# Kernel tuning notes

Measured on AMD Instinct MI355X. Metric: run time of the kernel, lower is better.

Reference implementation:

```python
import jax, jax.numpy as jnp
import numpy as np

EPS = 1.0        # model eps for norm
STEP = 0.05      # step_size

def _norm(x):
    # torch: x / (eps + x.std(-1, keepdims=True)), torch std is unbiased (ddof=1)
    return x / (EPS + jnp.std(x, axis=-1, keepdims=True, ddof=1))

def setup_inputs() -> dict:
    key = jax.random.key(0)
    B, L, LM = 4, 512, 64
    G, E, K, D, KN = 32000, 256, 8, 6, 4
    ks = jax.random.split(key, 16)
    s = lambda k, shape, fan: (jax.random.normal(k, shape, jnp.float32) / np.sqrt(fan)).astype(jnp.float32)
    return dict(
        masked=jax.random.randint(ks[0], (B, L), 0, G),
        unmasked=jax.random.randint(ks[1], (B, L), 0, G),
        mask=jax.random.randint(ks[2], (B, LM), 0, L),
        embed=s(ks[3], (G, E), E),                 # embedding table
        Wt=s(ks[4], (D, E, E), E),                 # transition.weight per layer
        bt=jnp.zeros((D, E), jnp.float32),         # transition.bias per layer
        Wtc=s(ks[5], (D, E, E), E),                # transcore.weight per layer
        Wq=s(ks[6], (D, K * E, E), E),             # attq.weight per layer
        Wd=s(ks[7], (D, K * E, K * E), K * E),     # att_dense.weight per layer
        Wo=s(ks[8], (D, K * E, E), K * E),         # atto.weight per layer
        Wu=s(ks[9], (D, E, E), E),                 # updater.weight per layer
        Wem=s(ks[10], (E, E), E),                  # emittor.weight (head)
        Wkc=s(ks[11], (E * KN, E), E),             # kchoice.weight (head)
        bkc=jnp.zeros((E * KN,), jnp.float32),     # kchoice.bias (head)
    )

def reference(masked, unmasked, mask, embed, Wt, bt, Wtc, Wq, Wd, Wo, Wu, Wem, Wkc, bkc):
    B, L = masked.shape
    G, E = embed.shape
    K = Wq.shape[1] // E
    KN = Wkc.shape[0] // E
    inv_sqrt_e = 1.0 / np.sqrt(E)

    z = _norm(embed[masked])          # [B,L,E] input image
    xsa0 = z

    def step(xsa, p):
        wt, bt_, wtc, wq, wd, wo, wu = p
        # roll-based left/right transitions
        xsad = jax.nn.relu(jnp.roll(xsa, 1, axis=1) @ wt) @ wtc
        xsad = xsad + jax.nn.relu(jnp.roll(xsa, -1, axis=1) @ wtc.T) @ wt.T
        xsad = xsad + z @ wu.T + bt_   # use_input_image
        # QKV_Attention with kernel-expanded head dim: q [B,L,K,E] vs keys/values xsa [B,L,E]
        q = (xsa @ wq.T).reshape(B, L, K, E)
        h = jnp.einsum('blke,bme->blkm', q, xsa) * inv_sqrt_e
        pijk = jax.nn.softmax(h, axis=-1)
        y = jnp.einsum('blkm,bme->blke', pijk, xsa).reshape(B, L, K * E)
        # mode 1: Dense -> Relu -> Dense
        xid = jax.nn.relu(y @ wd.T) @ wo     # [B,L,E]
        xsad = _norm(xsad + xid)             # use_gradnorm
        xsa = _norm(xsa + STEP * xsad)       # use_layernorm
        return xsa, None

    xsa, _ = jax.lax.scan(step, xsa0, (Wt, bt, Wtc, Wq, Wd, Wo, Wu))

    # k-choice loss head (callback_cent)
    LM = mask.shape[1]
    lptok = jnp.take_along_axis(xsa, mask[:, :, None], axis=1)         # [B,LM,E]
    xx = (lptok @ Wkc.T + bkc).reshape(B, LM * KN, E)                  # kchoice
    xx = jnp.einsum('bnl,ble->bne', jnp.einsum('bne,ble->bnl', xx, xsa), xsa)
    logits = (xx @ Wem) @ embed.T                                      # [B,LM*KN,G]
    k_lp = jax.nn.log_softmax(logits, axis=-1).reshape(B, LM, KN, G)
    lptok = jax.scipy.special.logsumexp(k_lp, axis=2) - jnp.log(jnp.float32(KN))
    tgt = jnp.take_along_axis(unmasked, mask, axis=1)                  # [B,LM]
    cent = jnp.take_along_axis(lptok, tgt[:, :, None], axis=-1)[:, :, 0]
    return -cent.mean(-1)                                              # [B]
```

## Files before the change

kernel.cpp:

```cpp
#include <hip/hip_runtime.h>
#include <hip/hip_bf16.h>
#include <math.h>

typedef __bf16 bf16x8 __attribute__((ext_vector_type(8)));
typedef float floatx4 __attribute__((ext_vector_type(4)));

__device__ __forceinline__ short f2b(float f) {
  __hip_bfloat16 h = __float2bfloat16(f);
  return *reinterpret_cast<short*>(&h);
}
__device__ __forceinline__ float b2f(short s) {
  unsigned u = ((unsigned)(unsigned short)s) << 16;
  float f;
  __builtin_memcpy(&f, &u, 4);
  return f;
}

__device__ __forceinline__ void gl2lds16(const void* g, void* l) {
  __builtin_amdgcn_global_load_lds((__attribute__((address_space(1))) const void*)g,
                                   (__attribute__((address_space(3))) void*)l, 16, 0, 0);
}

__device__ __forceinline__ float block_sum(float v, float* sdata) {
#pragma unroll
  for (int o = 32; o > 0; o >>= 1) v += __shfl_down(v, o, 64);
  __syncthreads();
  int lane = threadIdx.x & 63, wid = threadIdx.x >> 6;
  if (lane == 0) sdata[wid] = v;
  __syncthreads();
  float s = 0.f;
  int nw = blockDim.x >> 6;
  for (int i = 0; i < nw; i++) s += sdata[i];
  return s;
}

__global__ void cvt_kernel(const float* __restrict__ src, short* __restrict__ dst, long n4) {
  long i = (long)blockIdx.x * blockDim.x + threadIdx.x;
  if (i < n4) {
    float4 v = ((const float4*)src)[i];
    short4 o;
    o.x = f2b(v.x); o.y = f2b(v.y); o.z = f2b(v.z); o.w = f2b(v.w);
    ((short4*)dst)[i] = o;
  }
}

__global__ void cvt2_kernel(const float* __restrict__ src, short* __restrict__ dst,
                            int ldS, int ldD, long sS, long sD) {
  src += (size_t)blockIdx.z * sS;
  dst += (size_t)blockIdx.z * sD;
  int c = blockIdx.x * 32 + threadIdx.x;
  int r0 = blockIdx.y * 32 + threadIdx.y;
#pragma unroll
  for (int i = 0; i < 32; i += 8)
    dst[(size_t)(r0 + i) * ldD + c] = f2b(src[(size_t)(r0 + i) * ldS + c]);
}

__global__ void cvtT2_kernel(const float* __restrict__ src, short* __restrict__ dst,
                             int ldS, int ldD, long sS, long sD) {
  src += (size_t)blockIdx.z * sS;
  dst += (size_t)blockIdx.z * sD;
  __shared__ float tile[32][33];
  int r0 = blockIdx.y * 32, c0 = blockIdx.x * 32;
  int tx = threadIdx.x, ty = threadIdx.y;
#pragma unroll
  for (int i = 0; i < 32; i += 8)
    tile[ty + i][tx] = src[(size_t)(r0 + ty + i) * ldS + c0 + tx];
  __syncthreads();
#pragma unroll
  for (int i = 0; i < 32; i += 8)
    dst[(size_t)(c0 + ty + i) * ldD + r0 + tx] = f2b(tile[tx][ty + i]);
}

__global__ void embed_norm_kernel(const int* __restrict__ masked,
                                  const float* __restrict__ embed,
                                  float* __restrict__ xsa, short* __restrict__ xsa_bf,
                                  short* __restrict__ xsaT_bf, short* __restrict__ t3,
                                  int E, int L) {
  int row = blockIdx.x;
  int g = masked[row];
  __shared__ float sdata[8];
  float x = embed[(size_t)g * E + threadIdx.x];
  float mean = block_sum(x, sdata) / E;
  float d = x - mean;
  float var = block_sum(d * d, sdata) / (E - 1);
  float val = x / (1.0f + sqrtf(var));
  size_t off = (size_t)row * E + threadIdx.x;
  xsa[off] = val;
  short b = f2b(val);
  xsa_bf[off] = b;
  t3[(size_t)row * 3 * E + 2 * E + threadIdx.x] = b;
  int bb = row / L, l = row - bb * L;
  xsaT_bf[((size_t)bb * E + threadIdx.x) * L + l] = b;
}

template <int BM, int BN, int OUT_BF16>
__global__ __launch_bounds__(256) void bgemm_kernel(
    const short* __restrict__ A, int lda, long sA,
    const short* __restrict__ B, int ldb, long sB,
    void* __restrict__ Cv, int ldc, long sC,
    int Ksz, float alpha, const float* __restrict__ bias,
    int relu, int shiftA, int shiftB, int nsplit, int Lroll) {
  constexpr int WM = BM / 2, WN = BN / 2;
  constexpr int MT = WM / 16, NT = WN / 16;
  constexpr int NCH = (BM + BN) * 8;
  constexpr int LPT = NCH / 256;
  A += (size_t)blockIdx.z * sA;
  B += (size_t)blockIdx.z * sB;
  float* Cf = (float*)Cv + (size_t)blockIdx.z * sC;
  short* Cb = (short*)Cv + (size_t)blockIdx.z * sC;
  int m0 = blockIdx.y * BM, n0 = blockIdx.x * BN;
  int shift = (n0 < nsplit) ? shiftA : shiftB;
  __shared__ short S[2][(BM + BN) * 64];
  int tid = threadIdx.x, lane = tid & 63, w = tid >> 6;
  int wm = (w & 1) * WM, wn = (w >> 1) * WN;
  int ml = lane & 15, q4 = lane >> 4, sw = ml & 7;

  const short* src[LPT];
#pragma unroll
  for (int i = 0; i < LPT; i++) {
    int q = i * 256 + w * 64 + lane;
    if (q < BM * 8) {
      int m = q >> 3, cl = q & 7, cs = cl ^ (m & 7);
      int mg = m0 + m;
      if (shift != 0) {
        int bb = mg / Lroll, l = mg - bb * Lroll;
        l = (l + shift + Lroll) % Lroll;
        mg = bb * Lroll + l;
      }
      src[i] = A + (size_t)mg * lda + cs * 8;
    } else {
      int qb = q - BM * 8;
      int n = qb >> 3, cl = qb & 7, cs = cl ^ (n & 7);
      src[i] = B + (size_t)(n0 + n) * ldb + cs * 8;
    }
  }
#pragma unroll
  for (int i = 0; i < LPT; i++)
    gl2lds16(src[i], &S[0][(i * 256 + w * 64) * 8]);
  floatx4 acc[MT][NT] = {};
  int nT = Ksz >> 6;
  for (int t = 0; t < nT; t++) {
    __syncthreads();
    int cur = t & 1;
    if (t + 1 < nT) {
      int nxt = cur ^ 1, ko = (t + 1) * 64;
#pragma unroll
      for (int i = 0; i < LPT; i++)
        gl2lds16(src[i] + ko, &S[nxt][(i * 256 + w * 64) * 8]);
    }
#pragma unroll
    for (int kk = 0; kk < 2; kk++) {
      int j = kk * 4 + q4;
      bf16x8 af[MT], bg[NT];
#pragma unroll
      for (int mt = 0; mt < MT; mt++) {
        int r = wm + mt * 16 + ml;
        af[mt] = *reinterpret_cast<const bf16x8*>(&S[cur][r * 64 + (j ^ sw) * 8]);
      }
#pragma unroll
      for (int nt = 0; nt < NT; nt++) {
        int r = wn + nt * 16 + ml;
        bg[nt] = *reinterpret_cast<const bf16x8*>(&S[cur][BM * 64 + r * 64 + (j ^ sw) * 8]);
      }
#pragma unroll
      for (int mt = 0; mt < MT; mt++)
#pragma unroll
        for (int nt = 0; nt < NT; nt++)
          acc[mt][nt] = __builtin_amdgcn_mfma_f32_16x16x32_bf16(af[mt], bg[nt], acc[mt][nt], 0, 0, 0);
    }
  }
#pragma unroll
  for (int mt = 0; mt < MT; mt++)
#pragma unroll
    for (int nt = 0; nt < NT; nt++) {
      floatx4 v = acc[mt][nt];
#pragma unroll
      for (int r = 0; r < 4; r++) {
        int grow = m0 + wm + mt * 16 + q4 * 4 + r;
        int gcol = n0 + wn + nt * 16 + ml;
        float x = alpha * v[r];
        if (bias) x += bias[gcol];
        if (relu) x = fmaxf(x, 0.f);
        if (OUT_BF16)
          Cb[(size_t)grow * ldc + gcol] = f2b(x);
        else
          Cf[(size_t)grow * ldc + gcol] = x;
      }
    }
}

__global__ void softmax_bf_kernel(short* __restrict__ h) {
  int lane = threadIdx.x & 63;
  size_t row = (size_t)blockIdx.x * 4 + (threadIdx.x >> 6);
  short* p = h + row * 512 + lane * 8;
  int4 raw = *(const int4*)p;
  short sh[8];
  __builtin_memcpy(sh, &raw, 16);
  float v[8];
  float m = -INFINITY;
#pragma unroll
  for (int i = 0; i < 8; i++) {
    v[i] = b2f(sh[i]);
    m = fmaxf(m, v[i]);
  }
#pragma unroll
  for (int o = 1; o < 64; o <<= 1) m = fmaxf(m, __shfl_xor(m, o, 64));
  float s = 0.f;
#pragma unroll
  for (int i = 0; i < 8; i++) {
    v[i] = expf(v[i] - m);
    s += v[i];
  }
#pragma unroll
  for (int o = 1; o < 64; o <<= 1) s += __shfl_xor(s, o, 64);
  float inv = 1.f / s;
#pragma unroll
  for (int i = 0; i < 8; i++) sh[i] = f2b(v[i] * inv);
  __builtin_memcpy(&raw, sh, 16);
  *(int4*)p = raw;
}

__global__ void addnorm_kernel(const float* __restrict__ xsad,
                               const float* __restrict__ xid,
                               float* __restrict__ xsa, short* __restrict__ xsa_bf,
                               short* __restrict__ xsaT_bf, int E, int L) {
  int row = blockIdx.x, t = threadIdx.x;
  __shared__ float sdata[8];
  size_t off = (size_t)row * E + t;
  float s1 = xsad[off] + xid[off];
  float mean = block_sum(s1, sdata) / E;
  float d = s1 - mean;
  float var = block_sum(d * d, sdata) / (E - 1);
  float n1 = s1 / (1.f + sqrtf(var));
  float t2 = xsa[off] + 0.05f * n1;
  float mean2 = block_sum(t2, sdata) / E;
  float d2 = t2 - mean2;
  float var2 = block_sum(d2 * d2, sdata) / (E - 1);
  float res = t2 / (1.f + sqrtf(var2));
  xsa[off] = res;
  short b = f2b(res);
  xsa_bf[off] = b;
  int bb = row / L, l = row - bb * L;
  xsaT_bf[((size_t)bb * E + t) * L + l] = b;
}

__global__ void gather_kernel(const float* __restrict__ xsa, const int* __restrict__ mask,
                              const int* __restrict__ unmasked,
                              short* __restrict__ lptok_bf, int* __restrict__ tgt,
                              int L, int LM, int E) {
  int bi = blockIdx.x;
  int b = bi / LM;
  int pos = mask[bi];
  float v = xsa[((size_t)b * L + pos) * E + threadIdx.x];
  lptok_bf[(size_t)bi * E + threadIdx.x] = f2b(v);
  if (threadIdx.x == 0) tgt[bi] = unmasked[b * L + pos];
}

__global__ __launch_bounds__(256) void head_stats_kernel(
    const short* __restrict__ V, const short* __restrict__ Eb,
    float* __restrict__ stM, float* __restrict__ stS, int Ksz, int nch) {
  int m0 = blockIdx.y * 128, n0 = blockIdx.x * 128;
  __shared__ short As[2][8192];
  __shared__ short Bs[2][8192];
  int tid = threadIdx.x, lane = tid & 63, w = tid >> 6;
  int wm = (w & 1) * 64, wn = (w >> 1) * 64;
  int ml = lane & 15, q4 = lane >> 4, sw = ml & 7;
  const short* aSrc[4];
  const short* bSrc[4];
#pragma unroll
  for (int i = 0; i < 4; i++) {
    int q = i * 256 + w * 64 + lane;
    int m = q >> 3, cl = q & 7;
    int cs = cl ^ (m & 7);
    aSrc[i] = V + (size_t)(m0 + m) * Ksz + cs * 8;
    bSrc[i] = Eb + (size_t)(n0 + m) * Ksz + cs * 8;
  }
#pragma unroll
  for (int i = 0; i < 4; i++) {
    gl2lds16(aSrc[i], &As[0][(i * 256 + w * 64) * 8]);
    gl2lds16(bSrc[i], &Bs[0][(i * 256 + w * 64) * 8]);
  }
  floatx4 acc[4][4] = {};
  int nT = Ksz >> 6;
  for (int t = 0; t < nT; t++) {
    __syncthreads();
    int cur = t & 1;
    if (t + 1 < nT) {
      int nxt = cur ^ 1, ko = (t + 1) * 64;
#pragma unroll
      for (int i = 0; i < 4; i++) {
        gl2lds16(aSrc[i] + ko, &As[nxt][(i * 256 + w * 64) * 8]);
        gl2lds16(bSrc[i] + ko, &Bs[nxt][(i * 256 + w * 64) * 8]);
      }
    }
#pragma unroll
    for (int kk = 0; kk < 2; kk++) {
      int j = kk * 4 + q4;
      bf16x8 af[4], bg[4];
#pragma unroll
      for (int mt = 0; mt < 4; mt++) {
        int r = wm + mt * 16 + ml;
        af[mt] = *reinterpret_cast<const bf16x8*>(&As[cur][r * 64 + (j ^ sw) * 8]);
      }
#pragma unroll
      for (int nt = 0; nt < 4; nt++) {
        int r = wn + nt * 16 + ml;
        bg[nt] = *reinterpret_cast<const bf16x8*>(&Bs[cur][r * 64 + (j ^ sw) * 8]);
      }
#pragma unroll
      for (int mt = 0; mt < 4; mt++)
#pragma unroll
        for (int nt = 0; nt < 4; nt++)
          acc[mt][nt] = __builtin_amdgcn_mfma_f32_16x16x32_bf16(af[mt], bg[nt], acc[mt][nt], 0, 0, 0);
    }
  }
  __syncthreads();
  float (*sred)[2] = (float (*)[2]) & As[0][0];
  float (*sred2)[2] = (float (*)[2]) & Bs[0][0];
  float mx[4][4];
#pragma unroll
  for (int mt = 0; mt < 4; mt++)
#pragma unroll
    for (int r = 0; r < 4; r++)
      mx[mt][r] = fmaxf(fmaxf(acc[mt][0][r], acc[mt][1][r]), fmaxf(acc[mt][2][r], acc[mt][3][r]));
#pragma unroll
  for (int off = 1; off < 16; off <<= 1)
#pragma unroll
    for (int mt = 0; mt < 4; mt++)
#pragma unroll
      for (int r = 0; r < 4; r++) mx[mt][r] = fmaxf(mx[mt][r], __shfl_xor(mx[mt][r], off, 64));
  if (ml == 0)
#pragma unroll
    for (int mt = 0; mt < 4; mt++)
#pragma unroll
      for (int r = 0; r < 4; r++) sred[wm + mt * 16 + q4 * 4 + r][w >> 1] = mx[mt][r];
  __syncthreads();
  float sm[4][4];
#pragma unroll
  for (int mt = 0; mt < 4; mt++)
#pragma unroll
    for (int r = 0; r < 4; r++) {
      int row = wm + mt * 16 + q4 * 4 + r;
      float fm = fmaxf(sred[row][0], sred[row][1]);
      float s = 0.f;
#pragma unroll
      for (int nt = 0; nt < 4; nt++) s += expf(acc[mt][nt][r] - fm);
      sm[mt][r] = s;
    }
#pragma unroll
  for (int off = 1; off < 16; off <<= 1)
#pragma unroll
    for (int mt = 0; mt < 4; mt++)
#pragma unroll
      for (int r = 0; r < 4; r++) sm[mt][r] += __shfl_xor(sm[mt][r], off, 64);
  if (ml == 0)
#pragma unroll
    for (int mt = 0; mt < 4; mt++)
#pragma unroll
      for (int r = 0; r < 4; r++) sred2[wm + mt * 16 + q4 * 4 + r][w >> 1] = sm[mt][r];
  __syncthreads();
  if (tid < 128) {
    float fm = fmaxf(sred[tid][0], sred[tid][1]);
    stM[(size_t)(m0 + tid) * nch + blockIdx.x] = fm;
    stS[(size_t)(m0 + tid) * nch + blockIdx.x] = sred2[tid][0] + sred2[tid][1];
  }
}

__global__ void lse_reduce_kernel(const float* __restrict__ statsM,
                                  const float* __restrict__ statsS,
                                  float* __restrict__ lse, int nch) {
  int row = blockIdx.x, t = threadIdx.x;
  float m = -INFINITY, s = 0.f;
  for (int c = t; c < nch; c += blockDim.x) {
    float cm = statsM[(size_t)row * nch + c];
    float cs = statsS[(size_t)row * nch + c];
    float M = fmaxf(m, cm);
    s = s * expf(m - M) + cs * expf(cm - M);
    m = M;
  }
  __shared__ float sm[256], ss[256];
  sm[t] = m;
  ss[t] = s;
  __syncthreads();
  for (int o = 128; o > 0; o >>= 1) {
    if (t < o) {
      float m2 = sm[t + o], s2 = ss[t + o];
      float M = fmaxf(sm[t], m2);
      float sc = ss[t] * expf(sm[t] - M) + s2 * expf(m2 - M);
      sm[t] = M;
      ss[t] = sc;
    }
    __syncthreads();
  }
  if (t == 0) lse[row] = sm[0] + logf(ss[0]);
}

__global__ void logit_tgt_kernel(const short* __restrict__ V, const short* __restrict__ Eb,
                                 const int* __restrict__ tgt, float* __restrict__ lt,
                                 int E, int Nn, int KN, int LM) {
  int row = blockIdx.x;
  int b = row / Nn;
  int i = (row - b * Nn) / KN;
  int g = tgt[b * LM + i];
  __shared__ float sdata[8];
  float v = b2f(V[(size_t)row * E + threadIdx.x]) * b2f(Eb[(size_t)g * E + threadIdx.x]);
  float s = block_sum(v, sdata);
  if (threadIdx.x == 0) lt[row] = s;
}

__global__ void final_kernel(const float* __restrict__ lt, const float* __restrict__ lse,
                             float* __restrict__ out, int LM, int KN) {
  int b = blockIdx.x, i = threadIdx.x;
  int base = (b * LM + i) * KN;
  float m = -INFINITY;
  for (int k = 0; k < KN; k++) m = fmaxf(m, lt[base + k] - lse[base + k]);
  float s = 0.f;
  for (int k = 0; k < KN; k++) s += expf(lt[base + k] - lse[base + k] - m);
  float cent = m + logf(s) - logf((float)KN);
#pragma unroll
  for (int o = 32; o > 0; o >>= 1) cent += __shfl_down(cent, o, 64);
  if (i == 0) out[b] = -cent / LM;
}

static inline void bgemm(hipStream_t st, int cfg, const short* A, int lda, long sA,
                         const short* B, int ldb, long sB,
                         void* C, int ldc, long sC, int M, int N, int Ksz, int nb,
                         float alpha, const float* bias, int relu, int out_bf16,
                         int shiftA, int shiftB, int nsplit, int Lroll) {
  dim3 block(256);
  if (cfg == 0) {
    dim3 grid(N / 128, M / 128, nb);
    if (out_bf16)
      bgemm_kernel<128, 128, 1><<<grid, block, 0, st>>>(A, lda, sA, B, ldb, sB, C, ldc, sC, Ksz, alpha, bias, relu, shiftA, shiftB, nsplit, Lroll);
    else
      bgemm_kernel<128, 128, 0><<<grid, block, 0, st>>>(A, lda, sA, B, ldb, sB, C, ldc, sC, Ksz, alpha, bias, relu, shiftA, shiftB, nsplit, Lroll);
  } else if (cfg == 1) {
    dim3 grid(N / 64, M / 128, nb);
    if (out_bf16)
      bgemm_kernel<128, 64, 1><<<grid, block, 0, st>>>(A, lda, sA, B, ldb, sB, C, ldc, sC, Ksz, alpha, bias, relu, shiftA, shiftB, nsplit, Lroll);
    else
      bgemm_kernel<128, 64, 0><<<grid, block, 0, st>>>(A, lda, sA, B, ldb, sB, C, ldc, sC, Ksz, alpha, bias, relu, shiftA, shiftB, nsplit, Lroll);
  } else {
    dim3 grid(N / 64, M / 64, nb);
    if (out_bf16)
      bgemm_kernel<64, 64, 1><<<grid, block, 0, st>>>(A, lda, sA, B, ldb, sB, C, ldc, sC, Ksz, alpha, bias, relu, shiftA, shiftB, nsplit, Lroll);
    else
      bgemm_kernel<64, 64, 0><<<grid, block, 0, st>>>(A, lda, sA, B, ldb, sB, C, ldc, sC, Ksz, alpha, bias, relu, shiftA, shiftB, nsplit, Lroll);
  }
}

static inline void cvt(hipStream_t st, const float* src, short* dst, long n) {
  long n4 = n / 4;
  cvt_kernel<<<(int)((n4 + 255) / 256), 256, 0, st>>>(src, dst, n4);
}

static inline void cvt2(hipStream_t st, const float* src, short* dst, int R, int C,
                        int ldS, int ldD, long sS, long sD, int nb) {
  dim3 grid(C / 32, R / 32, nb), block(32, 8);
  cvt2_kernel<<<grid, block, 0, st>>>(src, dst, ldS, ldD, sS, sD);
}

static inline void cvtT2(hipStream_t st, const float* src, short* dst, int R, int C,
                         int ldS, int ldD, long sS, long sD, int nb) {
  dim3 grid(C / 32, R / 32, nb), block(32, 8);
  cvtT2_kernel<<<grid, block, 0, st>>>(src, dst, ldS, ldD, sS, sD);
}

extern "C" void kernel_launch(void* const* d_in, const int* in_sizes, int n_in,
                              void* d_out, int out_size, void* d_ws, size_t ws_size,
                              hipStream_t stream) {
  const int* masked = (const int*)d_in[0];
  const int* unmasked = (const int*)d_in[1];
  const int* mask = (const int*)d_in[2];
  const float* embed = (const float*)d_in[3];
  const float* Wt = (const float*)d_in[4];
  const float* bt = (const float*)d_in[5];
  const float* Wtc = (const float*)d_in[6];
  const float* Wq = (const float*)d_in[7];
  const float* Wd = (const float*)d_in[8];
  const float* Wo = (const float*)d_in[9];
  const float* Wu = (const float*)d_in[10];
  const float* Wem = (const float*)d_in[11];
  const float* Wkc = (const float*)d_in[12];
  const float* bkc = (const float*)d_in[13];

  const int B = out_size;
  const int BL = in_sizes[0];
  const int L = BL / B;
  const int BLM = in_sizes[2];
  const int LM = BLM / B;
  const int E = in_sizes[4] / in_sizes[5];
  const int D = in_sizes[5] / E;
  const int G = in_sizes[3] / E;
  const int K = in_sizes[7] / (D * E * E);
  const int KN = in_sizes[12] / (E * E);
  const int KE = K * E;
  const int N = LM * KN;
  const float inv_sqrt_e = 1.0f / sqrtf((float)E);
  const int nch = G / 128;
  const int E3 = 3 * E;

  char* base = (char*)d_ws;
  size_t off = 0;
  auto carve = [&](size_t bytes) {
    char* p = base + off;
    off += (bytes + 255) & ~(size_t)255;
    return p;
  };
  float* xsa = (float*)carve((size_t)BL * E * 4);
  float* xsad = (float*)carve((size_t)BL * E * 4);
  float* xid = (float*)carve((size_t)BL * E * 4);
  float* stM = (float*)carve((size_t)B * N * nch * 4);
  float* stS = (float*)carve((size_t)B * N * nch * 4);
  float* lse = (float*)carve((size_t)B * N * 4);
  float* lt = (float*)carve((size_t)B * N * 4);
  int* tgt = (int*)carve((size_t)B * LM * 4);
  short* xsa_bf = (short*)carve((size_t)BL * E * 2);
  short* xsaT_bf = (short*)carve((size_t)B * E * L * 2);
  short* t3 = (short*)carve((size_t)BL * E3 * 2);
  short* qy_bf = (short*)carve((size_t)BL * KE * 2);
  short* hP_bf = (short*)carve((size_t)B * L * K * L * 2);
  short* r_bf = hP_bf;
  short* wd_all = (short*)carve((size_t)D * KE * KE * 2);
  short* wq_all = (short*)carve((size_t)D * KE * E * 2);
  short* woT_all = (short*)carve((size_t)D * E * KE * 2);
  short* Bcat1 = (short*)carve((size_t)D * 2 * E * E * 2);
  short* Bcat2 = (short*)carve((size_t)D * E * E3 * 2);
  short* embed_bf = (short*)carve((size_t)G * E * 2);
  short* WemT_bf = (short*)carve((size_t)E * E * 2);
  short* Wkc_bf = (short*)carve((size_t)KN * E * E * 2);
  short* gram_bf = (short*)carve((size_t)B * E * E * 2);
  short* xx_bf = (short*)carve((size_t)B * N * E * 2);
  short* xx2_bf = (short*)carve((size_t)B * N * E * 2);
  short* vv_bf = (short*)carve((size_t)B * N * E * 2);
  short* lptok_bf = (short*)carve((size_t)BLM * E * 2);

  cvt(stream, embed, embed_bf, (long)G * E);
  cvt(stream, Wd, wd_all, (long)D * KE * KE);
  cvt(stream, Wq, wq_all, (long)D * KE * E);
  cvt(stream, Wkc, Wkc_bf, (long)KN * E * E);
  cvtT2(stream, Wem, WemT_bf, E, E, E, E, 0, 0, 1);
  cvtT2(stream, Wo, woT_all, KE, E, E, KE, (long)KE * E, (long)E * KE, D);
  cvtT2(stream, Wt, Bcat1, E, E, E, E, (long)E * E, (long)2 * E * E, D);
  cvt2(stream, Wtc, Bcat1 + (size_t)E * E, E, E, E, E, (long)E * E, (long)2 * E * E, D);
  cvtT2(stream, Wtc, Bcat2, E, E, E, E3, (long)E * E, (long)E * E3, D);
  cvt2(stream, Wt, Bcat2 + E, E, E, E, E3, (long)E * E, (long)E * E3, D);
  cvt2(stream, Wu, Bcat2 + 2 * E, E, E, E, E3, (long)E * E, (long)E * E3, D);

  embed_norm_kernel<<<BL, E, 0, stream>>>(masked, embed, xsa, xsa_bf, xsaT_bf, t3, E, L);

  for (int d = 0; d < D; d++) {
    const float* btl = bt + (size_t)d * E;
    bgemm(stream, 2, xsa_bf, E, 0, Bcat1 + (size_t)d * 2 * E * E, E, 0,
          t3, E3, 0, BL, 2 * E, E, 1, 1.f, nullptr, 1, 1, -1, +1, E, L);
    bgemm(stream, 2, t3, E3, 0, Bcat2 + (size_t)d * E * E3, E3, 0,
          xsad, E, 0, BL, E, E3, 1, 1.f, btl, 0, 0, 0, 0, 0, L);
    bgemm(stream, 1, xsa_bf, E, 0, wq_all + (size_t)d * KE * E, E, 0,
          qy_bf, KE, 0, BL, KE, E, 1, 1.f, nullptr, 0, 1, 0, 0, 0, L);
    bgemm(stream, 0, qy_bf, E, (long)L * KE, xsa_bf, E, (long)L * E,
          hP_bf, L, (long)L * K * L, L * K, L, E, B, inv_sqrt_e, nullptr, 0, 1, 0, 0, 0, L);
    softmax_bf_kernel<<<B * L * K / 4, 256, 0, stream>>>(hP_bf);
    bgemm(stream, 1, hP_bf, L, (long)L * K * L, xsaT_bf, L, (long)E * L,
          qy_bf, E, (long)L * KE, L * K, E, L, B, 1.f, nullptr, 0, 1, 0, 0, 0, L);
    bgemm(stream, 1, qy_bf, KE, 0, wd_all + (size_t)d * KE * KE, KE, 0,
          r_bf, KE, 0, BL, KE, KE, 1, 1.f, nullptr, 1, 1, 0, 0, 0, L);
    bgemm(stream, 2, r_bf, KE, 0, woT_all + (size_t)d * E * KE, KE, 0,
          xid, E, 0, BL, E, KE, 1, 1.f, nullptr, 0, 0, 0, 0, 0, L);
    addnorm_kernel<<<BL, E, 0, stream>>>(xsad, xid, xsa, xsa_bf, xsaT_bf, E, L);
  }

  gather_kernel<<<BLM, E, 0, stream>>>(xsa, mask, unmasked, lptok_bf, tgt, L, LM, E);
  bgemm(stream, 2, xsaT_bf, L, (long)E * L, xsaT_bf, L, (long)E * L,
        gram_bf, E, (long)E * E, E, E, L, B, 1.f, nullptr, 0, 1, 0, 0, 0, L);
  bgemm(stream, 2, lptok_bf, E, 0, Wkc_bf, E, 0, xx_bf, KN * E, 0, BLM, KN * E, E, 1,
        1.f, bkc, 0, 1, 0, 0, 0, L);
  bgemm(stream, 2, xx_bf, E, (long)N * E, gram_bf, E, (long)E * E,
        xx2_bf, E, (long)N * E, N, E, E, B, 1.f, nullptr, 0, 1, 0, 0, 0, L);
  bgemm(stream, 2, xx2_bf, E, 0, WemT_bf, E, 0, vv_bf, E, 0, B * N, E, E, 1,
        1.f, nullptr, 0, 1, 0, 0, 0, L);
  head_stats_kernel<<<dim3(nch, (B * N) / 128), 256, 0, stream>>>(vv_bf, embed_bf, stM, stS, E, nch);
  lse_reduce_kernel<<<B * N, 256, 0, stream>>>(stM, stS, lse, nch);
  logit_tgt_kernel<<<B * N, E, 0, stream>>>(vv_bf, embed_bf, tgt, lt, E, N, KN, LM);
  final_kernel<<<B, LM, 0, stream>>>(lt, lse, (float*)d_out, LM, KN);
}
```

Measured before the change: 946.9 us.

## Fuse attention QK^T, softmax and PV into a flash-style kernel; merge conversion kernels

Replaces the separate score GEMM, bf16 softmax pass and PV GEMM with one flash-attention kernel. It keeps Q fragments in registers, streams K and V tiles into LDS, applies an online softmax and writes the output in place over Q. This removes the large B*L*K*L score buffer and its global round trips, and avoids the bf16 rounding of the scores before softmax. The weight conversion kernels are also merged into one flat multi-tensor converter and one fused transpose/concat kernel to cut launch count. The flash kernel's V tile and P tile loads are serialized with several barriers, so it may not overlap well.

```diff
diff --git a/kernel.cpp b/kernel.cpp
--- a/kernel.cpp
+++ b/kernel.cpp
@@ -34,25 +34,23 @@
   return s;
 }
 
-__global__ void cvt_kernel(const float* __restrict__ src, short* __restrict__ dst, long n4) {
+__global__ void cvt4_kernel(const float* __restrict__ s0, short* __restrict__ d0, long n0,
+                            const float* __restrict__ s1, short* __restrict__ d1, long n1,
+                            const float* __restrict__ s2, short* __restrict__ d2, long n2,
+                            const float* __restrict__ s3, short* __restrict__ d3, long n3) {
   long i = (long)blockIdx.x * blockDim.x + threadIdx.x;
-  if (i < n4) {
-    float4 v = ((const float4*)src)[i];
-    short4 o;
-    o.x = f2b(v.x); o.y = f2b(v.y); o.z = f2b(v.z); o.w = f2b(v.w);
-    ((short4*)dst)[i] = o;
-  }
-}
-
-__global__ void cvt2_kernel(const float* __restrict__ src, short* __restrict__ dst,
-                            int ldS, int ldD, long sS, long sD) {
-  src += (size_t)blockIdx.z * sS;
-  dst += (size_t)blockIdx.z * sD;
-  int c = blockIdx.x * 32 + threadIdx.x;
-  int r0 = blockIdx.y * 32 + threadIdx.y;
-#pragma unroll
-  for (int i = 0; i < 32; i += 8)
-    dst[(size_t)(r0 + i) * ldD + c] = f2b(src[(size_t)(r0 + i) * ldS + c]);
+  const float* s;
+  short* d;
+  long j;
+  if (i < n0) { s = s0; d = d0; j = i; }
+  else if (i < n0 + n1) { s = s1; d = d1; j = i - n0; }
+  else if (i < n0 + n1 + n2) { s = s2; d = d2; j = i - n0 - n1; }
+  else if (i < n0 + n1 + n2 + n3) { s = s3; d = d3; j = i - n0 - n1 - n2; }
+  else return;
+  float4 v = ((const float4*)s)[j];
+  short4 o;
+  o.x = f2b(v.x); o.y = f2b(v.y); o.z = f2b(v.z); o.w = f2b(v.w);
+  ((short4*)d)[j] = o;
 }
 
 __global__ void cvtT2_kernel(const float* __restrict__ src, short* __restrict__ dst,
@@ -69,6 +67,35 @@
 #pragma unroll
   for (int i = 0; i < 32; i += 8)
     dst[(size_t)(c0 + ty + i) * ldD + r0 + tx] = f2b(tile[tx][ty + i]);
+}
+
+__global__ void prep_trans_kernel(const float* __restrict__ Wt, const float* __restrict__ Wtc,
+                                  const float* __restrict__ Wu,
+                                  short* __restrict__ Bcat1, short* __restrict__ Bcat2, int E) {
+  int d = blockIdx.z;
+  const float* wt = Wt + (size_t)d * E * E;
+  const float* wtc = Wtc + (size_t)d * E * E;
+  const float* wu = Wu + (size_t)d * E * E;
+  short* b1 = Bcat1 + (size_t)d * 2 * E * E;
+  short* b2 = Bcat2 + (size_t)d * E * 3 * E;
+  int E3 = 3 * E;
+  __shared__ float t1[32][33], t2[32][33];
+  int r0 = blockIdx.y * 32, c0 = blockIdx.x * 32;
+  int tx = threadIdx.x, ty = threadIdx.y;
+#pragma unroll
+  for (int i = 0; i < 32; i += 8) {
+    t1[ty + i][tx] = wt[(size_t)(r0 + ty + i) * E + c0 + tx];
+    t2[ty + i][tx] = wtc[(size_t)(r0 + ty + i) * E + c0 + tx];
+  }
+  __syncthreads();
+#pragma unroll
+  for (int i = 0; i < 32; i += 8) {
+    b1[(size_t)(c0 + ty + i) * E + r0 + tx] = f2b(t1[tx][ty + i]);
+    b1[(size_t)(E + r0 + ty + i) * E + c0 + tx] = f2b(t2[ty + i][tx]);
+    b2[(size_t)(c0 + ty + i) * E3 + r0 + tx] = f2b(t2[tx][ty + i]);
+    b2[(size_t)(r0 + ty + i) * E3 + E + c0 + tx] = f2b(t1[ty + i][tx]);
+    b2[(size_t)(r0 + ty + i) * E3 + 2 * E + c0 + tx] = f2b(wu[(size_t)(r0 + ty + i) * E + c0 + tx]);
+  }
 }
 
 __global__ void embed_norm_kernel(const int* __restrict__ masked,
@@ -189,35 +216,154 @@
     }
 }
 
-__global__ void softmax_bf_kernel(short* __restrict__ h) {
-  int lane = threadIdx.x & 63;
-  size_t row = (size_t)blockIdx.x * 4 + (threadIdx.x >> 6);
-  short* p = h + row * 512 + lane * 8;
-  int4 raw = *(const int4*)p;
-  short sh[8];
-  __builtin_memcpy(sh, &raw, 16);
-  float v[8];
-  float m = -INFINITY;
+__global__ __launch_bounds__(256) void flash_kernel(
+    short* __restrict__ Qy, const short* __restrict__ Kx, const short* __restrict__ Vt,
+    float scale, int L, int E, int KH) {
+  int b = blockIdx.y;
+  int LK = L * KH;
+  short* Q = Qy + (size_t)b * LK * E;
+  const short* Kb = Kx + (size_t)b * L * E;
+  const short* Vb = Vt + (size_t)b * E * L;
+  int qr0 = blockIdx.x * 64;
+
+  __shared__ short Ks[64 * 256];
+  __shared__ short Vs[256 * 32];
+  __shared__ short Ps[4][16 * 64];
+
+  int tid = threadIdx.x, lane = tid & 63, w = tid >> 6;
+  int ml = lane & 15, q4 = lane >> 4;
+
 #pragma unroll
   for (int i = 0; i < 8; i++) {
-    v[i] = b2f(sh[i]);
-    m = fmaxf(m, v[i]);
-  }
-#pragma unroll
-  for (int o = 1; o < 64; o <<= 1) m = fmaxf(m, __shfl_xor(m, o, 64));
-  float s = 0.f;
+    int q = i * 256 + tid;
+    int m = q >> 5, ec = q & 31;
+    int ecs = (ec & 24) | ((ec & 7) ^ (m & 7));
+    gl2lds16(Q + (size_t)(qr0 + m) * E + ecs * 8, &Ks[(i * 256 + w * 64) * 8]);
+  }
+  __syncthreads();
+  bf16x8 qf[8];
+#pragma unroll
+  for (int kk = 0; kk < 8; kk++) {
+    int ec = kk * 4 + q4;
+    qf[kk] = *reinterpret_cast<const bf16x8*>(
+        &Ks[(w * 16 + ml) * 256 + (ec & 24) * 8 + (((ec & 7) ^ (ml & 7))) * 8]);
+  }
+  __syncthreads();
+
+  const short* kSrc[8];
 #pragma unroll
   for (int i = 0; i < 8; i++) {
-    v[i] = expf(v[i] - m);
-    s += v[i];
-  }
-#pragma unroll
-  for (int o = 1; o < 64; o <<= 1) s += __shfl_xor(s, o, 64);
-  float inv = 1.f / s;
-#pragma unroll
-  for (int i = 0; i < 8; i++) sh[i] = f2b(v[i] * inv);
-  __builtin_memcpy(&raw, sh, 16);
-  *(int4*)p = raw;
+    int q = i * 256 + tid;
+    int m = q >> 5, ec = q & 31;
+    int ecs = (ec & 24) | ((ec & 7) ^ (m & 7));
+    kSrc[i] = Kb + (size_t)m * E + ecs * 8;
+  }
+  const short* vSrc[4];
+#pragma unroll
+  for (int i = 0; i < 4; i++) {
+    int q = i * 256 + tid;
+    int e = q >> 2, cl = q & 3;
+    int kc = cl ^ (e & 3);
+    vSrc[i] = Vb + (size_t)e * L + kc * 8;
+  }
+
+#pragma unroll
+  for (int i = 0; i < 8; i++) gl2lds16(kSrc[i], &Ks[(i * 256 + w * 64) * 8]);
+#pragma unroll
+  for (int i = 0; i < 4; i++) gl2lds16(vSrc[i], &Vs[(i * 256 + w * 64) * 8]);
+
+  floatx4 oacc[16] = {};
+  float mrun[4] = {-INFINITY, -INFINITY, -INFINITY, -INFINITY};
+  float lrun[4] = {0.f, 0.f, 0.f, 0.f};
+
+  int nTiles = L / 64;
+  for (int t = 0; t < nTiles; t++) {
+    __syncthreads();
+    floatx4 sacc[4] = {};
+#pragma unroll
+    for (int kk = 0; kk < 8; kk++) {
+      int ec = kk * 4 + q4;
+#pragma unroll
+      for (int nt = 0; nt < 4; nt++) {
+        int kr = nt * 16 + ml;
+        bf16x8 bf = *reinterpret_cast<const bf16x8*>(
+            &Ks[kr * 256 + (ec & 24) * 8 + (((ec & 7) ^ (ml & 7))) * 8]);
+        sacc[nt] = __builtin_amdgcn_mfma_f32_16x16x32_bf16(qf[kk], bf, sacc[nt], 0, 0, 0);
+      }
+    }
+    __syncthreads();
+    if (t + 1 < nTiles) {
+      int ko = (t + 1) * 64 * E;
+#pragma unroll
+      for (int i = 0; i < 8; i++) gl2lds16(kSrc[i] + ko, &Ks[(i * 256 + w * 64) * 8]);
+    }
+#pragma unroll
+    for (int r = 0; r < 4; r++) {
+      float mx = fmaxf(fmaxf(sacc[0][r], sacc[1][r]), fmaxf(sacc[2][r], sacc[3][r]));
+#pragma unroll
+      for (int o = 1; o < 16; o <<= 1) mx = fmaxf(mx, __shfl_xor(mx, o, 64));
+      float mnew = fmaxf(mrun[r], mx * scale);
+      float alpha = expf(mrun[r] - mnew);
+      mrun[r] = mnew;
+      lrun[r] *= alpha;
+#pragma unroll
+      for (int nto = 0; nto < 16; nto++) oacc[nto][r] *= alpha;
+      int mrow = q4 * 4 + r;
+      float s = 0.f;
+#pragma unroll
+      for (int nt = 0; nt < 4; nt++) {
+        float p = expf(sacc[nt][r] * scale - mnew);
+        s += p;
+        int col = nt * 16 + ml;
+        int cc = col >> 3;
+        Ps[w][mrow * 64 + ((cc ^ (mrow & 7))) * 8 + (col & 7)] = f2b(p);
+      }
+#pragma unroll
+      for (int o = 1; o < 16; o <<= 1) s += __shfl_xor(s, o, 64);
+      lrun[r] += s;
+    }
+    {
+      int cc = q4;
+      bf16x8 pf = *reinterpret_cast<const bf16x8*>(&Ps[w][ml * 64 + ((cc ^ (ml & 7))) * 8]);
+#pragma unroll
+      for (int nto = 0; nto < 16; nto++) {
+        int e = nto * 16 + ml;
+        bf16x8 vf = *reinterpret_cast<const bf16x8*>(&Vs[e * 32 + ((q4 ^ (e & 3))) * 8]);
+        oacc[nto] = __builtin_amdgcn_mfma_f32_16x16x32_bf16(pf, vf, oacc[nto], 0, 0, 0);
+      }
+    }
+    __syncthreads();
+    {
+      int ko = t * 64 + 32;
+#pragma unroll
+      for (int i = 0; i < 4; i++) gl2lds16(vSrc[i] + ko, &Vs[(i * 256 + w * 64) * 8]);
+    }
+    __syncthreads();
+    {
+      int cc = 4 + q4;
+      bf16x8 pf = *reinterpret_cast<const bf16x8*>(&Ps[w][ml * 64 + ((cc ^ (ml & 7))) * 8]);
+#pragma unroll
+      for (int nto = 0; nto < 16; nto++) {
+        int e = nto * 16 + ml;
+        bf16x8 vf = *reinterpret_cast<const bf16x8*>(&Vs[e * 32 + ((q4 ^ (e & 3))) * 8]);
+        oacc[nto] = __builtin_amdgcn_mfma_f32_16x16x32_bf16(pf, vf, oacc[nto], 0, 0, 0);
+      }
+    }
+    if (t + 1 < nTiles) {
+      __syncthreads();
+      int ko = (t + 1) * 64;
+#pragma unroll
+      for (int i = 0; i < 4; i++) gl2lds16(vSrc[i] + ko, &Vs[(i * 256 + w * 64) * 8]);
+    }
+  }
+#pragma unroll
+  for (int r = 0; r < 4; r++) {
+    float inv = 1.f / lrun[r];
+    int grow = qr0 + w * 16 + q4 * 4 + r;
+#pragma unroll
+    for (int nto = 0; nto < 16; nto++)
+      Q[(size_t)grow * E + nto * 16 + ml] = f2b(oacc[nto][r] * inv);
+  }
 }
 
 __global__ void addnorm_kernel(const float* __restrict__ xsad,
@@ -449,17 +595,6 @@
   }
 }
 
-static inline void cvt(hipStream_t st, const float* src, short* dst, long n) {
-  long n4 = n / 4;
-  cvt_kernel<<<(int)((n4 + 255) / 256), 256, 0, st>>>(src, dst, n4);
-}
-
-static inline void cvt2(hipStream_t st, const float* src, short* dst, int R, int C,
-                        int ldS, int ldD, long sS, long sD, int nb) {
-  dim3 grid(C / 32, R / 32, nb), block(32, 8);
-  cvt2_kernel<<<grid, block, 0, st>>>(src, dst, ldS, ldD, sS, sD);
-}
-
 static inline void cvtT2(hipStream_t st, const float* src, short* dst, int R, int C,
                          int ldS, int ldD, long sS, long sD, int nb) {
   dim3 grid(C / 32, R / 32, nb), block(32, 8);
@@ -519,8 +654,7 @@
   short* xsaT_bf = (short*)carve((size_t)B * E * L * 2);
   short* t3 = (short*)carve((size_t)BL * E3 * 2);
   short* qy_bf = (short*)carve((size_t)BL * KE * 2);
-  short* hP_bf = (short*)carve((size_t)B * L * K * L * 2);
-  short* r_bf = hP_bf;
+  short* r_bf = (short*)carve((size_t)BL * KE * 2);
   short* wd_all = (short*)carve((size_t)D * KE * KE * 2);
   short* wq_all = (short*)carve((size_t)D * KE * E * 2);
   short* woT_all = (short*)carve((size_t)D * E * KE * 2);
@@ -535,17 +669,19 @@
   short* vv_bf = (short*)carve((size_t)B * N * E * 2);
   short* lptok_bf = (short*)carve((size_t)BLM * E * 2);
 
-  cvt(stream, embed, embed_bf, (long)G * E);
-  cvt(stream, Wd, wd_all, (long)D * KE * KE);
-  cvt(stream, Wq, wq_all, (long)D * KE * E);
-  cvt(stream, Wkc, Wkc_bf, (long)KN * E * E);
+  {
+    long n0 = (long)G * E / 4, n1 = (long)D * KE * KE / 4;
+    long n2 = (long)D * KE * E / 4, n3 = (long)KN * E * E / 4;
+    long tot = n0 + n1 + n2 + n3;
+    cvt4_kernel<<<(int)((tot + 255) / 256), 256, 0, stream>>>(
+        embed, embed_bf, n0, Wd, wd_all, n1, Wq, wq_all, n2, Wkc, Wkc_bf, n3);
+  }
   cvtT2(stream, Wem, WemT_bf, E, E, E, E, 0, 0, 1);
   cvtT2(stream, Wo, woT_all, KE, E, E, KE, (long)KE * E, (long)E * KE, D);
-  cvtT2(stream, Wt, Bcat1, E, E, E, E, (long)E * E, (long)2 * E * E, D);
-  cvt2(stream, Wtc, Bcat1 + (size_t)E * E, E, E, E, E, (long)E * E, (long)2 * E * E, D);
-  cvtT2(stream, Wtc, Bcat2, E, E, E, E3, (long)E * E, (long)E * E3, D);
-  cvt2(stream, Wt, Bcat2 + E, E, E, E, E3, (long)E * E, (long)E * E3, D);
-  cvt2(stream, Wu, Bcat2 + 2 * E, E, E, E, E3, (long)E * E, (long)E * E3, D);
+  {
+    dim3 grid(E / 32, E / 32, D), block(32, 8);
+    prep_trans_kernel<<<grid, block, 0, stream>>>(Wt, Wtc, Wu, Bcat1, Bcat2, E);
+  }
 
   embed_norm_kernel<<<BL, E, 0, stream>>>(masked, embed, xsa, xsa_bf, xsaT_bf, t3, E, L);
 
@@ -557,11 +693,10 @@
           xsad, E, 0, BL, E, E3, 1, 1.f, btl, 0, 0, 0, 0, 0, L);
     bgemm(stream, 1, xsa_bf, E, 0, wq_all + (size_t)d * KE * E, E, 0,
           qy_bf, KE, 0, BL, KE, E, 1, 1.f, nullptr, 0, 1, 0, 0, 0, L);
-    bgemm(stream, 0, qy_bf, E, (long)L * KE, xsa_bf, E, (long)L * E,
-          hP_bf, L, (long)L * K * L, L * K, L, E, B, inv_sqrt_e, nullptr, 0, 1, 0, 0, 0, L);
-    softmax_bf_kernel<<<B * L * K / 4, 256, 0, stream>>>(hP_bf);
-    bgemm(stream, 1, hP_bf, L, (long)L * K * L, xsaT_bf, L, (long)E * L,
-          qy_bf, E, (long)L * KE, L * K, E, L, B, 1.f, nullptr, 0, 1, 0, 0, 0, L);
+    {
+      dim3 grid(L * K / 64, B), block(256);
+      flash_kernel<<<grid, block, 0, stream>>>(qy_bf, xsa_bf, xsaT_bf, inv_sqrt_e, L, E, K);
+    }
     bgemm(stream, 1, qy_bf, KE, 0, wd_all + (size_t)d * KE * KE, KE, 0,
           r_bf, KE, 0, BL, KE, KE, 1, 1.f, nullptr, 1, 1, 0, 0, 0, L);
     bgemm(stream, 2, r_bf, KE, 0, woT_all + (size_t)d * E * KE, KE, 0,
```

Measured after the change: 955.2 us. About the same (+0.9%).
